# Optimization experiments

Measured on AMD Instinct MI355X. Metric: run time of the kernel, lower is better.

## Reference

```python
import jax, jax.numpy as jnp
import numpy as np


def binarize_weight(w, scale=True):
    # Per-output-row mean-abs scale (dim=1 of [out, in]) times sign.
    # sign(0) -> 0 matches torch.sign semantics.
    s = jnp.mean(jnp.abs(w), axis=1, keepdims=True) if scale else jnp.ones((w.shape[0], 1), w.dtype)
    return jnp.sign(w) * s


def setup_inputs() -> dict:
    key = jax.random.key(0)
    kx, kw = jax.random.split(key)
    B, S, D_IN, D_OUT = 4, 2048, 4096, 4096
    x = jax.random.normal(kx, (B, S, D_IN), dtype=jnp.float32)
    # kaiming_normal_ with nonlinearity='linear': std = 1/sqrt(fan_in)
    weight = jax.random.normal(kw, (D_OUT, D_IN), dtype=jnp.float32) * (1.0 / np.sqrt(D_IN))
    return {"x": x, "weight": weight}


def reference(x, weight):
    w_b = binarize_weight(weight, scale=True)  # [out, in]
    # F.linear(x, w_b): x @ w_b.T
    return jnp.einsum("bsi,oi->bso", x, w_b)
```

## Files before the change

kernel.cpp:

```cpp
#include <hip/hip_runtime.h>
#include <hip/hip_bf16.h>
#include <stdint.h>

typedef int  iv4   __attribute__((ext_vector_type(4)));
typedef float f32x4 __attribute__((ext_vector_type(4)));

#define K_DIM 4096
#define N_DIM 4096
#define BKB   128

__global__ __launch_bounds__(256) void convert_x_i8(const float* __restrict__ x,
                                                    char* __restrict__ xq,
                                                    float* __restrict__ sx) {
    const int row = blockIdx.x;
    const int tid = threadIdx.x;
    const float* xr = x + (long long)row * K_DIM + tid * 16;

    float4 v0 = *(const float4*)(xr + 0);
    float4 v1 = *(const float4*)(xr + 4);
    float4 v2 = *(const float4*)(xr + 8);
    float4 v3 = *(const float4*)(xr + 12);

    float m = fabsf(v0.x);
    m = fmaxf(m, fabsf(v0.y)); m = fmaxf(m, fabsf(v0.z)); m = fmaxf(m, fabsf(v0.w));
    m = fmaxf(m, fabsf(v1.x)); m = fmaxf(m, fabsf(v1.y)); m = fmaxf(m, fabsf(v1.z)); m = fmaxf(m, fabsf(v1.w));
    m = fmaxf(m, fabsf(v2.x)); m = fmaxf(m, fabsf(v2.y)); m = fmaxf(m, fabsf(v2.z)); m = fmaxf(m, fabsf(v2.w));
    m = fmaxf(m, fabsf(v3.x)); m = fmaxf(m, fabsf(v3.y)); m = fmaxf(m, fabsf(v3.z)); m = fmaxf(m, fabsf(v3.w));

    #pragma unroll
    for (int d = 32; d > 0; d >>= 1) m = fmaxf(m, __shfl_xor(m, d));
    __shared__ float red[4];
    const int lane = tid & 63, wid = tid >> 6;
    if (lane == 0) red[wid] = m;
    __syncthreads();
    float rmax = fmaxf(fmaxf(red[0], red[1]), fmaxf(red[2], red[3]));
    rmax = fmaxf(rmax, 1e-20f);
    if (tid == 0) sx[row] = rmax * (1.0f / 127.0f);

    const float q = 127.0f / rmax;
    union { char c[16]; int4 v; } u;
    const float vals[16] = {v0.x, v0.y, v0.z, v0.w, v1.x, v1.y, v1.z, v1.w,
                            v2.x, v2.y, v2.z, v2.w, v3.x, v3.y, v3.z, v3.w};
    #pragma unroll
    for (int i = 0; i < 16; ++i) u.c[i] = (char)__float2int_rn(vals[i] * q);
    *(int4*)(xq + (long long)row * K_DIM + tid * 16) = u.v;
}

__global__ __launch_bounds__(256) void convert_w_i8(const float* __restrict__ w,
                                                    char* __restrict__ wq,
                                                    float* __restrict__ sw) {
    const int row = blockIdx.x;
    const int tid = threadIdx.x;
    const float* wr = w + (long long)row * K_DIM + tid * 16;

    float sum = 0.f;
    union { char c[16]; int4 v; } u;
    #pragma unroll
    for (int j = 0; j < 4; ++j) {
        float4 v = *(const float4*)(wr + j * 4);
        sum += fabsf(v.x) + fabsf(v.y) + fabsf(v.z) + fabsf(v.w);
        u.c[j * 4 + 0] = (char)((v.x > 0.f) - (v.x < 0.f));
        u.c[j * 4 + 1] = (char)((v.y > 0.f) - (v.y < 0.f));
        u.c[j * 4 + 2] = (char)((v.z > 0.f) - (v.z < 0.f));
        u.c[j * 4 + 3] = (char)((v.w > 0.f) - (v.w < 0.f));
    }
    *(int4*)(wq + (long long)row * K_DIM + tid * 16) = u.v;

    #pragma unroll
    for (int d = 32; d > 0; d >>= 1) sum += __shfl_down(sum, d);
    __shared__ float red[4];
    const int lane = tid & 63, wid = tid >> 6;
    if (lane == 0) red[wid] = sum;
    __syncthreads();
    if (tid == 0) sw[row] = (red[0] + red[1] + red[2] + red[3]) * (1.0f / (float)K_DIM);
}

struct SOp { const char* g; int row0; int kt; char* l; };

__device__ __forceinline__ void stage_half(const SOp s, int wid, int lane) {
    const int srcsw = ((lane & 7) ^ ((lane >> 3) & 7)) << 4;
    #pragma unroll
    for (int op = 0; op < 2; ++op) {
        const int r = s.row0 + wid * 16 + op * 8 + (lane >> 3);
        const char* src = s.g + (long long)r * K_DIM + s.kt + srcsw;
        __builtin_amdgcn_global_load_lds(
            (const __attribute__((address_space(1))) void*)src,
            (__attribute__((address_space(3))) void*)(s.l + wid * 2048 + op * 1024),
            16, 0, 0);
    }
}

__device__ __forceinline__ iv4 ldsr(const char* t, int row, int slot) {
    return *(const iv4*)(t + row * 128 + ((slot ^ (row & 7)) << 4));
}

__device__ __forceinline__ void read_ah(iv4 (&a)[4][2], const char* tA,
                                        int wm, int h, int l15, int c) {
    #pragma unroll
    for (int mi = 0; mi < 4; ++mi)
        #pragma unroll
        for (int kk = 0; kk < 2; ++kk)
            a[mi][kk] = ldsr(tA, wm * 128 + h * 64 + mi * 16 + l15, kk * 4 + c);
}
__device__ __forceinline__ void read_bv(iv4 (&b)[2][2], const char* tB,
                                        int wn, int v, int l15, int c) {
    #pragma unroll
    for (int ni = 0; ni < 2; ++ni)
        #pragma unroll
        for (int kk = 0; kk < 2; ++kk)
            b[ni][kk] = ldsr(tB, wn * 64 + v * 32 + ni * 16 + l15, kk * 4 + c);
}

template<int H, int V>
__device__ __forceinline__ void mfma_q(iv4 (&acc)[8][4],
                                       const iv4 (&a)[4][2], const iv4 (&b)[2][2]) {
    #pragma unroll
    for (int kk = 0; kk < 2; ++kk)
        #pragma unroll
        for (int mi = 0; mi < 4; ++mi)
            #pragma unroll
            for (int ni = 0; ni < 2; ++ni)
                acc[H * 4 + mi][V * 2 + ni] = __builtin_amdgcn_mfma_i32_16x16x64_i8(
                    a[mi][kk], b[ni][kk], acc[H * 4 + mi][V * 2 + ni], 0, 0, 0);
}

template<bool S0, bool S1, bool S2, bool S3, int WN>
__device__ __forceinline__ void ktile(const char* __restrict__ cA,
                                      const char* __restrict__ cB,
                                      char* __restrict__ oA,
                                      char* __restrict__ oB,
                                      char* __restrict__ curA,
                                      const char* gA, const char* gB,
                                      int ktn, int ktn2,
                                      iv4 (&acc)[8][4],
                                      int wm, int wn, int wid, int lane)
{
    const int l15 = lane & 15;
    const int c   = lane >> 4;
    iv4 a[4][2], b0[2][2], b1[2][2];

    read_ah(a, cA, wm, 0, l15, c);
    read_bv(b0, cB, wn, 0, l15, c);
    if constexpr (S0) stage_half({gA, 128, ktn, oA + 16384}, wid, lane);
    __builtin_amdgcn_s_barrier();
    __builtin_amdgcn_s_setprio(1);
    mfma_q<0, 0>(acc, a, b0);
    __builtin_amdgcn_s_setprio(0);
    __builtin_amdgcn_s_barrier();

    read_bv(b1, cB, wn, 1, l15, c);
    if constexpr (S1) stage_half({gB, 0, ktn, oB}, wid, lane);
    __builtin_amdgcn_s_barrier();
    __builtin_amdgcn_s_setprio(1);
    mfma_q<0, 1>(acc, a, b1);
    __builtin_amdgcn_s_setprio(0);
    __builtin_amdgcn_s_barrier();

    read_ah(a, cA, wm, 1, l15, c);
    if constexpr (S2) stage_half({gB, 128, ktn, oB + 16384}, wid, lane);
    __builtin_amdgcn_s_barrier();
    __builtin_amdgcn_s_setprio(1);
    mfma_q<1, 1>(acc, a, b1);
    __builtin_amdgcn_s_setprio(0);
    __builtin_amdgcn_s_barrier();

    if constexpr (S3) stage_half({gA, 0, ktn2, curA}, wid, lane);
    __builtin_amdgcn_s_barrier();
    __builtin_amdgcn_s_setprio(1);
    mfma_q<1, 0>(acc, a, b0);
    __builtin_amdgcn_s_setprio(0);
    if constexpr (WN == 2)      asm volatile("s_waitcnt vmcnt(2)" ::: "memory");
    else if constexpr (WN == 0) asm volatile("s_waitcnt vmcnt(0)" ::: "memory");
    if constexpr (WN >= 0) __builtin_amdgcn_s_barrier();
}

__global__ __launch_bounds__(512, 2) void bitlinear_gemm_i8(
    const char* __restrict__ A, const char* __restrict__ B,
    const float* __restrict__ sx, const float* __restrict__ sw,
    float* __restrict__ C, int M)
{
    extern __shared__ char smem[];
    char* As0 = smem;
    char* As1 = smem + 32768;
    char* Bs0 = smem + 65536;
    char* Bs1 = smem + 98304;

    const int tid = threadIdx.x, lane = tid & 63, wid = tid >> 6;
    const int wm = wid >> 2, wn = wid & 3;

    const int nbid = (int)blockIdx.x;
    const int cpx  = (int)gridDim.x >> 3;
    const int swz  = (nbid & 7) * cpx + (nbid >> 3);
    const int ntn  = N_DIM / 256;
    const int tm = swz / ntn, tn = swz % ntn;

    const char* gA = A + (long long)tm * 256 * K_DIM;
    const char* gB = B + (long long)tn * 256 * K_DIM;

    iv4 acc[8][4];
    #pragma unroll
    for (int i = 0; i < 8; ++i)
        #pragma unroll
        for (int j = 0; j < 4; ++j) acc[i][j] = (iv4){0, 0, 0, 0};

    stage_half({gA,   0,   0, As0},         wid, lane);
    stage_half({gA, 128,   0, As0 + 16384}, wid, lane);
    stage_half({gB,   0,   0, Bs0},         wid, lane);
    stage_half({gB, 128,   0, Bs0 + 16384}, wid, lane);
    stage_half({gA,   0, BKB, As1},         wid, lane);
    asm volatile("s_waitcnt vmcnt(2)" ::: "memory");
    __builtin_amdgcn_s_barrier();

    ktile<true, true, true, true, 2>(As0, Bs0, As1, Bs1, As0,
                                     gA, gB, 1 * BKB, 2 * BKB,
                                     acc, wm, wn, wid, lane);
    #pragma unroll 1
    for (int i = 0; i < 14; ++i) {
        const int t = 2 * i + 1;
        ktile<true, true, true, true, 2>(As1, Bs1, As0, Bs0, As1,
                                         gA, gB, (t + 1) * BKB, (t + 2) * BKB,
                                         acc, wm, wn, wid, lane);
        ktile<true, true, true, true, 2>(As0, Bs0, As1, Bs1, As0,
                                         gA, gB, (t + 2) * BKB, (t + 3) * BKB,
                                         acc, wm, wn, wid, lane);
    }
    ktile<true, true, true, true, 2>(As1, Bs1, As0, Bs0, As1,
                                     gA, gB, 30 * BKB, 31 * BKB,
                                     acc, wm, wn, wid, lane);
    ktile<true, true, true, false, 0>(As0, Bs0, As1, Bs1, As0,
                                      gA, gB, 31 * BKB, 0,
                                      acc, wm, wn, wid, lane);
    ktile<false, false, false, false, -1>(As1, Bs1, As0, Bs0, As1,
                                          gA, gB, 0, 0,
                                          acc, wm, wn, wid, lane);

    const long long m0 = (long long)tm * 256 + wm * 128;
    const long long n0 = (long long)tn * 256 + wn * 64;
    float swv[4];
    #pragma unroll
    for (int ni = 0; ni < 4; ++ni) swv[ni] = sw[n0 + ni * 16 + (lane & 15)];
    #pragma unroll
    for (int mi = 0; mi < 8; ++mi) {
        const long long rowb = m0 + mi * 16 + (lane >> 4) * 4;
        float sxr[4];
        #pragma unroll
        for (int j = 0; j < 4; ++j) sxr[j] = sx[rowb + j];
        #pragma unroll
        for (int ni = 0; ni < 4; ++ni) {
            const long long col = n0 + ni * 16 + (lane & 15);
            #pragma unroll
            for (int j = 0; j < 4; ++j)
                C[(rowb + j) * N_DIM + col] = (float)acc[mi][ni][j] * swv[ni] * sxr[j];
        }
    }
}

__global__ void bitlinear_naive_kernel(const float* __restrict__ x,
                                       const float* __restrict__ w,
                                       float* __restrict__ out, long long total) {
    const long long idx = (long long)blockIdx.x * blockDim.x + threadIdx.x;
    if (idx >= total) return;
    const long long m = idx / N_DIM;
    const long long o = idx % N_DIM;
    const float* xr = x + m * K_DIM;
    const float* wrow = w + o * K_DIM;
    float sum = 0.f, sa = 0.f;
    for (int k = 0; k < K_DIM; ++k) {
        float wv = wrow[k];
        sa += fabsf(wv);
        sum += xr[k] * ((wv > 0.f) ? 1.f : ((wv < 0.f) ? -1.f : 0.f));
    }
    out[idx] = sum * (sa * (1.0f / (float)K_DIM));
}

extern "C" void kernel_launch(void* const* d_in, const int* in_sizes, int n_in,
                              void* d_out, int out_size, void* d_ws, size_t ws_size,
                              hipStream_t stream) {
    const float* x = (const float*)d_in[0];
    const float* w = (const float*)d_in[1];
    float* out = (float*)d_out;

    const int M = in_sizes[0] / K_DIM;

    const size_t xq_bytes = (size_t)M * K_DIM;
    const size_t wq_bytes = (size_t)N_DIM * K_DIM;
    const size_t sx_bytes = (size_t)M * sizeof(float);
    const size_t sw_bytes = (size_t)N_DIM * sizeof(float);

    if (ws_size < xq_bytes + wq_bytes + sx_bytes + sw_bytes || (M % 256) != 0) {
        const long long total = (long long)M * N_DIM;
        bitlinear_naive_kernel<<<(int)((total + 255) / 256), 256, 0, stream>>>(x, w, out, total);
        return;
    }

    char*  xq = (char*)d_ws;
    char*  wq = (char*)d_ws + xq_bytes;
    float* sx = (float*)((char*)d_ws + xq_bytes + wq_bytes);
    float* sw = (float*)((char*)d_ws + xq_bytes + wq_bytes + sx_bytes);

    convert_x_i8<<<M, 256, 0, stream>>>(x, xq, sx);
    convert_w_i8<<<N_DIM, 256, 0, stream>>>(w, wq, sw);

    hipFuncSetAttribute((const void*)bitlinear_gemm_i8,
                        hipFuncAttributeMaxDynamicSharedMemorySize, 131072);
    const int grid = (M / 256) * (N_DIM / 256);
    bitlinear_gemm_i8<<<grid, 512, 131072, stream>>>(xq, wq, sx, sw, out, M);
}
```

Before: 173.3 us.

## Load B operand directly from global into registers, stage only A in LDS

B fragments are now read straight from global memory into registers each k-tile instead of being staged through LDS, and LDS holds only a double-buffered A tile (64 KB instead of 128 KB). The block-to-tile mapping is changed so each XCD group owns two fixed column tiles. This targets LDS traffic, LDS capacity and barrier overhead for B, and aims to improve L2 locality of B per XCD. In exchange, B loads are strided global accesses whose latency sits inside each k-tile, and they are duplicated across waves.

```diff
diff --git a/kernel.cpp b/kernel.cpp
--- a/kernel.cpp
+++ b/kernel.cpp
@@ -102,13 +102,19 @@
         for (int kk = 0; kk < 2; ++kk)
             a[mi][kk] = ldsr(tA, wm * 128 + h * 64 + mi * 16 + l15, kk * 4 + c);
 }
-__device__ __forceinline__ void read_bv(iv4 (&b)[2][2], const char* tB,
-                                        int wn, int v, int l15, int c) {
-    #pragma unroll
-    for (int ni = 0; ni < 2; ++ni)
+
+__device__ __forceinline__ void load_bv(iv4 (&b)[2][2], const char* gB,
+                                        int wn, int v, int kt, int lane) {
+    const int l15 = lane & 15;
+    const int co  = (lane >> 4) * 16;
+    #pragma unroll
+    for (int ni = 0; ni < 2; ++ni) {
+        const char* rowp = gB + (long long)(wn * 64 + v * 32 + ni * 16 + l15) * K_DIM
+                              + kt + co;
         #pragma unroll
         for (int kk = 0; kk < 2; ++kk)
-            b[ni][kk] = ldsr(tB, wn * 64 + v * 32 + ni * 16 + l15, kk * 4 + c);
+            b[ni][kk] = *(const iv4*)(rowp + kk * 64);
+    }
 }
 
 template<int H, int V>
@@ -124,14 +130,11 @@
                     a[mi][kk], b[ni][kk], acc[H * 4 + mi][V * 2 + ni], 0, 0, 0);
 }
 
-template<bool S0, bool S1, bool S2, bool S3, int WN>
+template<bool ST, bool WB>
 __device__ __forceinline__ void ktile(const char* __restrict__ cA,
-                                      const char* __restrict__ cB,
                                       char* __restrict__ oA,
-                                      char* __restrict__ oB,
-                                      char* __restrict__ curA,
                                       const char* gA, const char* gB,
-                                      int ktn, int ktn2,
+                                      int ktn, int kt,
                                       iv4 (&acc)[8][4],
                                       int wm, int wn, int wid, int lane)
 {
@@ -140,16 +143,16 @@
     iv4 a[4][2], b0[2][2], b1[2][2];
 
     read_ah(a, cA, wm, 0, l15, c);
-    read_bv(b0, cB, wn, 0, l15, c);
-    if constexpr (S0) stage_half({gA, 128, ktn, oA + 16384}, wid, lane);
+    load_bv(b0, gB, wn, 0, kt, lane);
+    load_bv(b1, gB, wn, 1, kt, lane);
+    if constexpr (ST) stage_half({gA, 0, ktn, oA}, wid, lane);
     __builtin_amdgcn_s_barrier();
     __builtin_amdgcn_s_setprio(1);
     mfma_q<0, 0>(acc, a, b0);
     __builtin_amdgcn_s_setprio(0);
     __builtin_amdgcn_s_barrier();
 
-    read_bv(b1, cB, wn, 1, l15, c);
-    if constexpr (S1) stage_half({gB, 0, ktn, oB}, wid, lane);
+    if constexpr (ST) stage_half({gA, 128, ktn, oA + 16384}, wid, lane);
     __builtin_amdgcn_s_barrier();
     __builtin_amdgcn_s_setprio(1);
     mfma_q<0, 1>(acc, a, b1);
@@ -157,21 +160,19 @@
     __builtin_amdgcn_s_barrier();
 
     read_ah(a, cA, wm, 1, l15, c);
-    if constexpr (S2) stage_half({gB, 128, ktn, oB + 16384}, wid, lane);
     __builtin_amdgcn_s_barrier();
     __builtin_amdgcn_s_setprio(1);
     mfma_q<1, 1>(acc, a, b1);
     __builtin_amdgcn_s_setprio(0);
     __builtin_amdgcn_s_barrier();
 
-    if constexpr (S3) stage_half({gA, 0, ktn2, curA}, wid, lane);
-    __builtin_amdgcn_s_barrier();
     __builtin_amdgcn_s_setprio(1);
     mfma_q<1, 0>(acc, a, b0);
     __builtin_amdgcn_s_setprio(0);
-    if constexpr (WN == 2)      asm volatile("s_waitcnt vmcnt(2)" ::: "memory");
-    else if constexpr (WN == 0) asm volatile("s_waitcnt vmcnt(0)" ::: "memory");
-    if constexpr (WN >= 0) __builtin_amdgcn_s_barrier();
+    if constexpr (WB) {
+        asm volatile("s_waitcnt vmcnt(0)" ::: "memory");
+        __builtin_amdgcn_s_barrier();
+    }
 }
 
 __global__ __launch_bounds__(512, 2) void bitlinear_gemm_i8(
@@ -182,57 +183,42 @@
     extern __shared__ char smem[];
     char* As0 = smem;
     char* As1 = smem + 32768;
-    char* Bs0 = smem + 65536;
-    char* Bs1 = smem + 98304;
 
     const int tid = threadIdx.x, lane = tid & 63, wid = tid >> 6;
     const int wm = wid >> 2, wn = wid & 3;
 
     const int nbid = (int)blockIdx.x;
-    const int cpx  = (int)gridDim.x >> 3;
-    const int swz  = (nbid & 7) * cpx + (nbid >> 3);
-    const int ntn  = N_DIM / 256;
-    const int tm = swz / ntn, tn = swz % ntn;
+    const int xcd  = nbid & 7;
+    const int i    = nbid >> 3;
+    const int tn   = 2 * xcd + (i & 1);
+    const int tm   = i >> 1;
 
     const char* gA = A + (long long)tm * 256 * K_DIM;
     const char* gB = B + (long long)tn * 256 * K_DIM;
 
     iv4 acc[8][4];
     #pragma unroll
-    for (int i = 0; i < 8; ++i)
-        #pragma unroll
-        for (int j = 0; j < 4; ++j) acc[i][j] = (iv4){0, 0, 0, 0};
-
-    stage_half({gA,   0,   0, As0},         wid, lane);
-    stage_half({gA, 128,   0, As0 + 16384}, wid, lane);
-    stage_half({gB,   0,   0, Bs0},         wid, lane);
-    stage_half({gB, 128,   0, Bs0 + 16384}, wid, lane);
-    stage_half({gA,   0, BKB, As1},         wid, lane);
-    asm volatile("s_waitcnt vmcnt(2)" ::: "memory");
-    __builtin_amdgcn_s_barrier();
-
-    ktile<true, true, true, true, 2>(As0, Bs0, As1, Bs1, As0,
-                                     gA, gB, 1 * BKB, 2 * BKB,
-                                     acc, wm, wn, wid, lane);
+    for (int ii = 0; ii < 8; ++ii)
+        #pragma unroll
+        for (int j = 0; j < 4; ++j) acc[ii][j] = (iv4){0, 0, 0, 0};
+
+    stage_half({gA,   0, 0, As0},         wid, lane);
+    stage_half({gA, 128, 0, As0 + 16384}, wid, lane);
+    asm volatile("s_waitcnt vmcnt(0)" ::: "memory");
+    __builtin_amdgcn_s_barrier();
+
     #pragma unroll 1
-    for (int i = 0; i < 14; ++i) {
-        const int t = 2 * i + 1;
-        ktile<true, true, true, true, 2>(As1, Bs1, As0, Bs0, As1,
-                                         gA, gB, (t + 1) * BKB, (t + 2) * BKB,
-                                         acc, wm, wn, wid, lane);
-        ktile<true, true, true, true, 2>(As0, Bs0, As1, Bs1, As0,
-                                         gA, gB, (t + 2) * BKB, (t + 3) * BKB,
-                                         acc, wm, wn, wid, lane);
-    }
-    ktile<true, true, true, true, 2>(As1, Bs1, As0, Bs0, As1,
-                                     gA, gB, 30 * BKB, 31 * BKB,
-                                     acc, wm, wn, wid, lane);
-    ktile<true, true, true, false, 0>(As0, Bs0, As1, Bs1, As0,
-                                      gA, gB, 31 * BKB, 0,
-                                      acc, wm, wn, wid, lane);
-    ktile<false, false, false, false, -1>(As1, Bs1, As0, Bs0, As1,
-                                          gA, gB, 0, 0,
-                                          acc, wm, wn, wid, lane);
+    for (int it = 0; it < 15; ++it) {
+        const int t = 2 * it;
+        ktile<true, true>(As0, As1, gA, gB, (t + 1) * BKB, t * BKB,
+                          acc, wm, wn, wid, lane);
+        ktile<true, true>(As1, As0, gA, gB, (t + 2) * BKB, (t + 1) * BKB,
+                          acc, wm, wn, wid, lane);
+    }
+    ktile<true, true>(As0, As1, gA, gB, 31 * BKB, 30 * BKB,
+                      acc, wm, wn, wid, lane);
+    ktile<false, false>(As1, As0, gA, gB, 0, 31 * BKB,
+                        acc, wm, wn, wid, lane);
 
     const long long m0 = (long long)tm * 256 + wm * 128;
     const long long n0 = (long long)tn * 256 + wn * 64;
@@ -302,7 +288,7 @@
     convert_w_i8<<<N_DIM, 256, 0, stream>>>(w, wq, sw);
 
     hipFuncSetAttribute((const void*)bitlinear_gemm_i8,
-                        hipFuncAttributeMaxDynamicSharedMemorySize, 131072);
+                        hipFuncAttributeMaxDynamicSharedMemorySize, 65536);
     const int grid = (M / 256) * (N_DIM / 256);
-    bitlinear_gemm_i8<<<grid, 512, 131072, stream>>>(xq, wq, sx, sw, out, M);
-}
+    bitlinear_gemm_i8<<<grid, 512, 65536, stream>>>(xq, wq, sx, sw, out, M);
+}
```

New measurement: 278.9 us. 1.61x slower.
